# Performance work log

Measured on AMD Instinct MI355X. Metric: run time of the kernel, lower is better.

Reference implementation:

```python
import jax, jax.numpy as jnp
import numpy as np

B, T, D = 32, 2048, 80
K1 = K2 = 3
S1 = S2 = 2
CB_DIM, CB_SIZE = 512, 1024
MASK_P = 0.1
NOISE_STD = 0.1
INPUT_DIM = D * K1 * K2  # 720


def _win_idx(T_in, k, s):
    Tp = (T_in - k) // s + 1
    return jnp.arange(Tp)[:, None] * s + jnp.arange(k)[None, :]  # (Tp, k)


def _unfold(x, k, s):
    # matches torch x.unfold(1, k, s).view(B, Tp, -1): out[b, t, f*k + j] = x[b, t*s + j, f]
    idx = _win_idx(x.shape[1], k, s)
    w = x[:, idx, :]                 # (B, Tp, k, F)
    w = jnp.swapaxes(w, 2, 3)        # (B, Tp, F, k)
    return w.reshape(w.shape[0], w.shape[1], -1)


def setup_inputs() -> dict:
    key = jax.random.key(0)
    k1, k2, k3, k4, k5 = jax.random.split(key, 5)
    raw_feats = jax.random.normal(k1, (B, T, D), jnp.float32)
    auged_feats = jax.random.normal(k2, (B, T, D), jnp.float32)
    length = jax.random.randint(k3, (B,), T // 2, T + 1)
    xav = (2.0 / (INPUT_DIM + CB_DIM)) ** 0.5  # xavier_normal std
    projector = jax.random.normal(k4, (INPUT_DIM, CB_DIM), jnp.float32) * xav
    codebook = jax.random.normal(k5, (CB_SIZE, CB_DIM), jnp.float32)
    return {"raw_feats": raw_feats, "auged_feats": auged_feats, "length": length,
            "projector": projector, "codebook": codebook}


def reference(raw_feats, auged_feats, length, projector, codebook):
    T1 = (T - K1) // S1 + 1
    T2 = (T1 - K2) // S2 + 1
    idx1 = _win_idx(T, K1, S1)                         # (T1, K1)
    idx2 = _win_idx(T1, K2, S2)                        # (T2, K2)
    frame_windows = idx1[idx2].reshape(T2, K1 * K2)    # (T2, 9) original frame idx per subsampled step
    label_lengths = ((length - K1) // S1 + 1 - K2) // S2 + 1  # (B,)

    # --- label path: two torch-style unfolds -> project -> nearest codebook entry ---
    stacked = _unfold(_unfold(raw_feats, K1, S1), K2, S2)     # (B, T2, 720)
    targets = jnp.matmul(stacked, projector)                  # (B, T2, 512)
    # squared-euclidean expansion; same argmin as ||t - c||
    dist = (jnp.sum(targets * targets, axis=-1, keepdims=True)
            - 2.0 * jnp.einsum('btd,cd->btc', targets, codebook)
            + jnp.sum(codebook * codebook, axis=-1))          # (B, T2, 1024)
    labels = jnp.argmin(dist, axis=-1) + 1                    # labels start from 1; 0 = ignore idx
    valid = jnp.arange(T2)[None, :] < label_lengths[:, None]  # (B, T2)
    labels = jnp.where(valid, labels, 0)[None]                # (num_codebooks=1, B, T2)

    # --- static (span length 1) random masking on valid subsampled steps ---
    mkey = jax.random.key(42)
    km, kn = jax.random.split(mkey)
    masked = (jax.random.uniform(km, (B, T2)) < MASK_P) & valid
    masked_dim = masked.astype(jnp.float32)                   # (B, T2)
    # scatter masked subsampled steps back onto original frame indices (union of windows)
    hits = jnp.zeros((B, T), jnp.float32).at[:, frame_windows].add(masked_dim[:, :, None])
    frame_mask = hits > 0                                     # (B, T)
    noise = NOISE_STD * jax.random.normal(kn, (B, T, D), auged_feats.dtype)
    masked_feats = jnp.where(frame_mask[:, :, None], noise, auged_feats)
    return masked_feats, labels, masked_dim
```

## Files before the change

### kernel.cpp

```cpp
#include <hip/hip_runtime.h>
#include <cstdint>

#define B_    32
#define T_    2048
#define D_    80
#define T2_   511
#define NROW  16352
#define GK    720
#define CBD   512
#define CBS   1024
#define HMASK 8176
#define HN    2621440
#define NP    16384
#define KB    23
#define GLDS  (259*81*4)

using bfrag = __attribute__((ext_vector_type(8))) short;
using f32x4 = __attribute__((ext_vector_type(4))) float;
using s8    = __attribute__((ext_vector_type(8))) short;

__device__ inline ushort f2bf(float f){
  uint32_t u = __float_as_uint(f);
  uint32_t r = (u + 0x7FFFu + ((u >> 16) & 1u)) >> 16;
  return (ushort)r;
}
__device__ inline float bf2f(ushort h){ return __uint_as_float(((uint32_t)h) << 16); }

#define GLL16(gsrc, ldst) __builtin_amdgcn_global_load_lds( \
    (__attribute__((address_space(1))) void*)(gsrc), \
    (__attribute__((address_space(3))) void*)(ldst), 16, 0, 0)

__host__ __device__ inline uint32_t rotl_(uint32_t v, int d){ return (v<<d)|(v>>(32-d)); }

__host__ __device__ inline void tf2x32(uint32_t k0, uint32_t k1, uint32_t& x0, uint32_t& x1){
  uint32_t ks2 = k0 ^ k1 ^ 0x1BD11BDAu;
  x0 += k0; x1 += k1;
  const int r0[4] = {13,15,26,6}, r1[4] = {17,29,16,24};
#pragma unroll
  for (int i=0;i<4;i++){ x0 += x1; x1 = rotl_(x1, r0[i]); x1 ^= x0; }
  x0 += k1; x1 += ks2 + 1u;
#pragma unroll
  for (int i=0;i<4;i++){ x0 += x1; x1 = rotl_(x1, r1[i]); x1 ^= x0; }
  x0 += ks2; x1 += k0 + 2u;
#pragma unroll
  for (int i=0;i<4;i++){ x0 += x1; x1 = rotl_(x1, r0[i]); x1 ^= x0; }
  x0 += k0; x1 += k1 + 3u;
#pragma unroll
  for (int i=0;i<4;i++){ x0 += x1; x1 = rotl_(x1, r1[i]); x1 ^= x0; }
  x0 += k1; x1 += ks2 + 4u;
#pragma unroll
  for (int i=0;i<4;i++){ x0 += x1; x1 = rotl_(x1, r0[i]); x1 ^= x0; }
  x0 += ks2; x1 += k0 + 5u;
}

__device__ inline float erfinv_f(float x){
  float w = -log1pf(-x*x);
  float p;
  if (w < 5.0f){
    w -= 2.5f;
    p = 2.81022636e-08f;
    p = fmaf(p, w, 3.43273939e-07f);
    p = fmaf(p, w, -3.5233877e-06f);
    p = fmaf(p, w, -4.39150654e-06f);
    p = fmaf(p, w, 0.00021858087f);
    p = fmaf(p, w, -0.00125372503f);
    p = fmaf(p, w, -0.00417768164f);
    p = fmaf(p, w, 0.246640727f);
    p = fmaf(p, w, 1.50140941f);
  } else {
    w = sqrtf(w) - 3.0f;
    p = -0.000200214257f;
    p = fmaf(p, w, 0.000100950558f);
    p = fmaf(p, w, 0.00134934322f);
    p = fmaf(p, w, -0.00367342844f);
    p = fmaf(p, w, 0.00573950773f);
    p = fmaf(p, w, -0.0076224613f);
    p = fmaf(p, w, 0.00943887047f);
    p = fmaf(p, w, 1.00167406f);
    p = fmaf(p, w, 2.83297682f);
  }
  return p * x;
}

__device__ inline int label_len(int L){ return (((L - 3) / 2) - 2) / 2 + 1; }

__global__ void cbnorm_k(const float* __restrict__ cb, ushort* __restrict__ W0, ushort* __restrict__ W1){
  int c = blockIdx.x, lane = threadIdx.x;
  double s = 0.0;
  for (int k = lane; k < CBD; k += 64){ float v = cb[c*CBD + k]; s += (double)v * (double)v; }
#pragma unroll
  for (int off = 32; off; off >>= 1) s += __shfl_down(s, off);
  float nf = (float)s;
  nf = __shfl(nf, 0);
  size_t base = ((size_t)(KB-1)*CBS + c)*32;
  int sw = ((c >> 1) & 3) << 3;
  if (lane == 16){
    float h = -0.5f * nf;
    ushort h0 = f2bf(h); ushort h1 = f2bf(h - bf2f(h0));
    W0[base + (16 ^ sw)] = h0; W1[base + (16 ^ sw)] = h1;
  } else if (lane > 16 && lane < 32){
    W0[base + (lane ^ sw)] = 0; W1[base + (lane ^ sw)] = 0;
  }
}

__global__ __launch_bounds__(256) void gather_k(const float* __restrict__ raw,
                                                ushort* __restrict__ S0, ushort* __restrict__ S1){
  extern __shared__ float lraw[];
  int b = blockIdx.x >> 3, ch = blockIdx.x & 7;
  int t20 = ch * 64;
  int nt2 = (T2_ - t20 < 64) ? (T2_ - t20) : 64;
  int r0 = 4 * t20;
  int rows = (T_ - r0 < 259) ? (T_ - r0) : 259;
  int tid = threadIdx.x;
  const float4* gsrc = (const float4*)(raw + ((size_t)b*T_ + r0)*D_);
  int nf4 = rows * 20;
  for (int q = tid; q < nf4; q += 256){
    float4 v = gsrc[q];
    int row = q / 20, c4 = (q - row*20) * 4;
    float* dst = &lraw[row*81 + c4];
    dst[0]=v.x; dst[1]=v.y; dst[2]=v.z; dst[3]=v.w;
  }
  __syncthreads();
  int nl = tid >> 2, g = tid & 3;
  if (nl >= nt2) return;
  int n = b*T2_ + t20 + nl;
  int gs = g ^ ((n >> 1) & 3);
  for (int kb = 0; kb < KB; ++kb){
    s8 o0, o1;
#pragma unroll
    for (int j = 0; j < 8; ++j){
      int k = kb*32 + g*8 + j;
      float v = 0.f;
      if (k < GK){
        int d = k / 9, rem = k - 9*d;
        int k1 = rem / 3, k2 = rem - 3*k1;
        v = lraw[(4*nl + 2*k2 + k1)*81 + d];
      } else if (k == GK) v = 1.f;
      ushort h0 = f2bf(v); ushort h1 = f2bf(v - bf2f(h0));
      o0[j] = (short)h0; o1[j] = (short)h1;
    }
    size_t off = ((size_t)kb*NP + n)*32 + gs*8;
    *(s8*)&S0[off] = o0;
    *(s8*)&S1[off] = o1;
  }
}

__global__ __launch_bounds__(256) void wgemm_k(const float* __restrict__ P, const float* __restrict__ cb,
                                               float* __restrict__ Wp){
  __shared__ float sP[16][68];
  __shared__ float sC[16][68];
  int r0 = blockIdx.y * 64, c0 = blockIdx.x * 64;
  int kz = blockIdx.z;
  int tid = threadIdx.x, tx = tid & 15, ty = tid >> 4;
  float acc[4][4] = {};
  for (int k0 = kz * 128; k0 < kz * 128 + 128; k0 += 16){
    __syncthreads();
    {
      int r = tid >> 2, kq = tid & 3;
      int rr = r0 + r;
      float4 v = {0.f,0.f,0.f,0.f};
      if (rr < GK) v = *(const float4*)&P[rr * CBD + k0 + kq * 4];
      sP[kq*4+0][r] = v.x; sP[kq*4+1][r] = v.y; sP[kq*4+2][r] = v.z; sP[kq*4+3][r] = v.w;
      float4 w = *(const float4*)&cb[(c0 + r) * CBD + k0 + kq * 4];
      sC[kq*4+0][r] = w.x; sC[kq*4+1][r] = w.y; sC[kq*4+2][r] = w.z; sC[kq*4+3][r] = w.w;
    }
    __syncthreads();
#pragma unroll
    for (int kk = 0; kk < 16; ++kk){
      float4 a = *(const float4*)&sP[kk][ty * 4];
      float4 b = *(const float4*)&sC[kk][tx * 4];
      float av[4] = {a.x,a.y,a.z,a.w}, bv[4] = {b.x,b.y,b.z,b.w};
#pragma unroll
      for (int i = 0; i < 4; ++i)
#pragma unroll
        for (int j = 0; j < 4; ++j) acc[i][j] = fmaf(av[i], bv[j], acc[i][j]);
    }
  }
#pragma unroll
  for (int i = 0; i < 4; ++i){
    int r = r0 + ty * 4 + i;
    if (r < GK){
      float4 o; o.x = acc[i][0]; o.y = acc[i][1]; o.z = acc[i][2]; o.w = acc[i][3];
      *(float4*)&Wp[((size_t)kz * GK + r) * CBS + c0 + tx * 4] = o;
    }
  }
}

__global__ void wreduce_k(const float* __restrict__ Wp, ushort* __restrict__ W0, ushort* __restrict__ W1){
  int idx = blockIdx.x * 256 + threadIdx.x;
  int r = idx >> 10, c = idx & (CBS - 1);
  float v = Wp[(size_t)r * CBS + c]
          + Wp[((size_t)GK + r) * CBS + c]
          + Wp[((size_t)2*GK + r) * CBS + c]
          + Wp[((size_t)3*GK + r) * CBS + c];
  ushort h0 = f2bf(v); ushort h1 = f2bf(v - bf2f(h0));
  size_t o = ((size_t)(r >> 5) * CBS + c) * 32 + ((r & 31) ^ (((c >> 1) & 3) << 3));
  W0[o] = h0; W1[o] = h1;
}

__global__ __launch_bounds__(512, 2) void score_k(const ushort* __restrict__ S0, const ushort* __restrict__ S1,
                                                  const ushort* __restrict__ W0, const ushort* __restrict__ W1,
                                                  float* __restrict__ pval, int* __restrict__ pidx){
  extern __shared__ ushort lds[];
  int tid = threadIdx.x;
  int lane = tid & 63, wid = tid >> 6;
  int wm = wid >> 2, wn = wid & 3;
  int g = lane >> 4, lr = lane & 15;
  int gsw = g ^ ((lr >> 1) & 3);

  int id = blockIdx.x;
  int xcd = id & 7, slot = id >> 3;
  int cidx = slot & 3, ridx = (xcd << 3) | (slot >> 2);
  int n0 = ridx * 256, c0 = cidx * 256;

  int p = wid >> 1, h = wid & 1;
  const ushort* src0;
  size_t kstride;
  if      (p == 0){ src0 = S0 + (size_t)n0*32; kstride = (size_t)NP*32; }
  else if (p == 1){ src0 = S1 + (size_t)n0*32; kstride = (size_t)NP*32; }
  else if (p == 2){ src0 = W0 + (size_t)c0*32; kstride = (size_t)CBS*32; }
  else            { src0 = W1 + (size_t)c0*32; kstride = (size_t)CBS*32; }
  src0 += h * 4096;
  int doff = p * 8192 + h * 4096;

  f32x4 acc[8][4] = {};

#pragma unroll
  for (int q = 0; q < 8; ++q) GLL16(src0 + q*512 + lane*8, lds + doff + q*512);

  int abase = (wm*128 + lr)*32 + gsw*8;
  int bbase = (wn*64  + lr)*32 + gsw*8;

  for (int kb = 0; kb < KB; ++kb){
    const ushort* cur = lds + (kb & 1) * 32768;
    ushort*       nxt = lds + ((kb & 1) ^ 1) * 32768;
    asm volatile("s_waitcnt vmcnt(0)" ::: "memory");
    __builtin_amdgcn_s_barrier();

    const ushort* A0 = cur;
    const ushort* A1 = cur + 8192;
    const ushort* B0 = cur + 16384;
    const ushort* B1 = cur + 24576;

    bfrag a[4], b0f[4], b1f[4];
#pragma unroll
    for (int mt = 0; mt < 4; ++mt) a[mt] = *(const bfrag*)&A0[abase + mt*512];
#pragma unroll
    for (int nt = 0; nt < 4; ++nt) b0f[nt] = *(const bfrag*)&B0[bbase + nt*512];
    if (kb + 1 < KB){
      const ushort* s = src0 + (size_t)(kb+1)*kstride;
#pragma unroll
      for (int q = 0; q < 8; ++q) GLL16(s + q*512 + lane*8, nxt + doff + q*512);
    }
    asm volatile("s_waitcnt lgkmcnt(0)" ::: "memory");
    __builtin_amdgcn_sched_barrier(0);
    __builtin_amdgcn_s_setprio(1);
#pragma unroll
    for (int mt = 0; mt < 4; ++mt)
#pragma unroll
      for (int nt = 0; nt < 4; ++nt)
        acc[mt][nt] = __builtin_amdgcn_mfma_f32_16x16x32_bf16(a[mt], b0f[nt], acc[mt][nt], 0,0,0);
    __builtin_amdgcn_s_setprio(0);
    __builtin_amdgcn_sched_barrier(0);
    __builtin_amdgcn_s_barrier();
#pragma unroll
    for (int nt = 0; nt < 4; ++nt) b1f[nt] = *(const bfrag*)&B1[bbase + nt*512];
    asm volatile("s_waitcnt lgkmcnt(0)" ::: "memory");
    __builtin_amdgcn_sched_barrier(0);
    __builtin_amdgcn_s_setprio(1);
#pragma unroll
    for (int mt = 0; mt < 4; ++mt)
#pragma unroll
      for (int nt = 0; nt < 4; ++nt)
        acc[mt][nt] = __builtin_amdgcn_mfma_f32_16x16x32_bf16(a[mt], b1f[nt], acc[mt][nt], 0,0,0);
    __builtin_amdgcn_s_setprio(0);
    __builtin_amdgcn_sched_barrier(0);
    __builtin_amdgcn_s_barrier();
#pragma unroll
    for (int mt = 0; mt < 4; ++mt) a[mt] = *(const bfrag*)&A0[abase + (mt+4)*512];
    asm volatile("s_waitcnt lgkmcnt(0)" ::: "memory");
    __builtin_amdgcn_sched_barrier(0);
    __builtin_amdgcn_s_setprio(1);
#pragma unroll
    for (int mt = 0; mt < 4; ++mt)
#pragma unroll
      for (int nt = 0; nt < 4; ++nt)
        acc[4+mt][nt] = __builtin_amdgcn_mfma_f32_16x16x32_bf16(a[mt], b0f[nt], acc[4+mt][nt], 0,0,0);
#pragma unroll
    for (int mt = 0; mt < 4; ++mt)
#pragma unroll
      for (int nt = 0; nt < 4; ++nt)
        acc[4+mt][nt] = __builtin_amdgcn_mfma_f32_16x16x32_bf16(a[mt], b1f[nt], acc[4+mt][nt], 0,0,0);
    __builtin_amdgcn_s_setprio(0);
    __builtin_amdgcn_sched_barrier(0);
    __builtin_amdgcn_s_barrier();
    bfrag a1f[8];
#pragma unroll
    for (int mt = 0; mt < 8; ++mt) a1f[mt] = *(const bfrag*)&A1[abase + mt*512];
    asm volatile("s_waitcnt lgkmcnt(0)" ::: "memory");
    __builtin_amdgcn_sched_barrier(0);
    __builtin_amdgcn_s_setprio(1);
#pragma unroll
    for (int mt = 0; mt < 8; ++mt)
#pragma unroll
      for (int nt = 0; nt < 4; ++nt)
        acc[mt][nt] = __builtin_amdgcn_mfma_f32_16x16x32_bf16(a1f[mt], b0f[nt], acc[mt][nt], 0,0,0);
    __builtin_amdgcn_s_setprio(0);
    __builtin_amdgcn_sched_barrier(0);
  }

#pragma unroll
  for (int mt = 0; mt < 8; ++mt){
    float bv[4]; int bi[4];
#pragma unroll
    for (int r = 0; r < 4; ++r){
      float best = 3.4e38f; int besti = 0;
#pragma unroll
      for (int nt = 0; nt < 4; ++nt){
        float d = -2.f * acc[mt][nt][r];
        int c = c0 + wn*64 + nt*16 + lr;
        if (d < best){ best = d; besti = c; }
      }
      bv[r] = best; bi[r] = besti;
    }
#pragma unroll
    for (int off = 1; off < 16; off <<= 1){
#pragma unroll
      for (int r = 0; r < 4; ++r){
        float ov = __shfl_xor(bv[r], off);
        int   oi = __shfl_xor(bi[r], off);
        if (ov < bv[r] || (ov == bv[r] && oi < bi[r])){ bv[r] = ov; bi[r] = oi; }
      }
    }
    if (lr == 0){
      int pp = cidx*4 + wn;
#pragma unroll
      for (int r = 0; r < 4; ++r){
        int n = n0 + wm*128 + mt*16 + g*4 + r;
        pval[(size_t)pp*NP + n] = bv[r];
        pidx[(size_t)pp*NP + n] = bi[r];
      }
    }
  }
}

__device__ inline void emit_mask(const int* len, float* md, int i, uint32_t bits){
  float u = __uint_as_float((bits >> 9) | 0x3F800000u) - 1.0f;
  int b = i / T2_, t2 = i - b * T2_;
  bool m = (u < 0.1f) && (t2 < label_len(len[b]));
  md[i] = m ? 1.0f : 0.0f;
}

__device__ inline void comb_one(const float* __restrict__ pval, const int* __restrict__ pidx,
                                const int* __restrict__ len, float* __restrict__ lb, int n){
  float bv = pval[n]; int bi = pidx[n];
#pragma unroll
  for (int p = 1; p < 16; ++p){
    float v = pval[(size_t)p*NP + n]; int ii = pidx[(size_t)p*NP + n];
    if (v < bv || (v == bv && ii < bi)){ bv = v; bi = ii; }
  }
  int b = n / T2_, t2 = n - b * T2_;
  lb[n] = (t2 < label_len(len[b])) ? (float)(bi + 1) : 0.f;
}

__global__ void maskcomb_k(const float* __restrict__ pval, const int* __restrict__ pidx,
                           const int* __restrict__ len, float* __restrict__ lb,
                           float* __restrict__ md, uint32_t km0, uint32_t km1){
  int j = blockIdx.x * 256 + threadIdx.x;
  if (j >= HMASK) return;
  uint32_t x0 = (uint32_t)j, x1 = (uint32_t)(j + HMASK);
  tf2x32(km0, km1, x0, x1);
  emit_mask(len, md, j, x0);
  emit_mask(len, md, j + HMASK, x1);
  comb_one(pval, pidx, len, lb, j);
  comb_one(pval, pidx, len, lb, j + HMASK);
}

__device__ inline bool frame_masked(const float* md, int i){
  int tabs = i / D_;
  int t = tabs & (T_ - 1);
  int b = i / (D_ * T_);
  int lo = (t < 3) ? 0 : ((t - 3) >> 2);
  int hi = t >> 2; if (hi > T2_ - 1) hi = T2_ - 1;
  bool m = false;
  for (int t2 = lo; t2 <= hi; ++t2) m = m || (md[b * T2_ + t2] != 0.f);
  return m;
}

__device__ inline float noise_from_bits(uint32_t bits){
  float f = __uint_as_float((bits >> 9) | 0x3F800000u) - 1.0f;
  const float LOV = -0.99999994f;
  float u = fmaf(f, 2.0f, LOV);
  u = fmaxf(LOV, u);
  return 0.1f * (1.41421356f * erfinv_f(u));
}

__global__ void feats_k(const float* __restrict__ aug, const float* __restrict__ md,
                        float* __restrict__ mf, uint32_t kn0, uint32_t kn1){
  int j = blockIdx.x * 256 + threadIdx.x;
  bool m1 = frame_masked(md, j);
  bool m2 = frame_masked(md, j + HN);
  if (m1 || m2){
    uint32_t x0 = (uint32_t)j, x1 = (uint32_t)(j + HN);
    tf2x32(kn0, kn1, x0, x1);
    mf[j]      = m1 ? noise_from_bits(x0) : aug[j];
    mf[j + HN] = m2 ? noise_from_bits(x1) : aug[j + HN];
  } else {
    mf[j]      = aug[j];
    mf[j + HN] = aug[j + HN];
  }
}

extern "C" void kernel_launch(void* const* d_in, const int* in_sizes, int n_in,
                              void* d_out, int out_size, void* d_ws, size_t ws_size,
                              hipStream_t stream){
  const float* raw  = (const float*)d_in[0];
  const float* aug  = (const float*)d_in[1];
  const int*   len  = (const int*)  d_in[2];
  const float* proj = (const float*)d_in[3];
  const float* cb   = (const float*)d_in[4];

  float* out = (float*)d_out;
  float* mf  = out;
  float* lb  = out + 5242880;
  float* md  = out + 5259232;

  ushort* w  = (ushort*)d_ws;
  ushort* W0 = w;
  ushort* W1 = W0 + (size_t)KB*CBS*32;
  ushort* S0 = W1 + (size_t)KB*CBS*32;
  ushort* S1 = S0 + (size_t)KB*NP*32;
  float* pval = (float*)(S1 + (size_t)KB*NP*32);
  int*   pidx = (int*)(pval + (size_t)16*NP);
  float* Wp   = (float*)(pidx + (size_t)16*NP);

  hipFuncSetAttribute((const void*)score_k,  hipFuncAttributeMaxDynamicSharedMemorySize, 131072);
  hipFuncSetAttribute((const void*)gather_k, hipFuncAttributeMaxDynamicSharedMemorySize, GLDS);

  uint32_t a0 = 0u, a1 = 2u, b0 = 1u, b1 = 3u;
  tf2x32(0u, 42u, a0, a1);
  tf2x32(0u, 42u, b0, b1);
  uint32_t km0 = a0, km1 = b0, kn0 = a1, kn1 = b1;

  cbnorm_k<<<CBS, 64, 0, stream>>>(cb, W0, W1);
  wgemm_k<<<dim3(CBS / 64, 12, 4), 256, 0, stream>>>(proj, cb, Wp);
  wreduce_k<<<(GK * CBS) / 256, 256, 0, stream>>>(Wp, W0, W1);
  gather_k<<<256, 256, GLDS, stream>>>(raw, S0, S1);
  score_k<<<256, 512, 131072, stream>>>(S0, S1, W0, W1, pval, pidx);
  maskcomb_k<<<(HMASK + 255) / 256, 256, 0, stream>>>(pval, pidx, len, lb, md, km0, km1);
  feats_k<<<HN / 256, 256, 0, stream>>>(aug, md, mf, kn0, kn1);
}
```

Baseline: 147.8 us.

## Restructure score_k pipeline with early prefetch and fold cbnorm into wreduce

The codebook-norm kernel is merged into wreduce_k as extra blocks, removing one kernel launch. In score_k, the next k-block's global-to-LDS prefetch is now issued at the top of each iteration, followed by a partial vmcnt wait. The per-phase barriers and lgkmcnt waits between MFMA groups are dropped, so LDS fragment reads interleave with the MFMA groups. This aims to overlap memory loads with compute and cut synchronisation stalls. It risks relying on the compiler to insert correct LDS waits and on the partial vmcnt count staying correct.

```diff
diff --git a/kernel.cpp b/kernel.cpp
--- a/kernel.cpp
+++ b/kernel.cpp
@@ -84,25 +84,6 @@
 
 __device__ inline int label_len(int L){ return (((L - 3) / 2) - 2) / 2 + 1; }
 
-__global__ void cbnorm_k(const float* __restrict__ cb, ushort* __restrict__ W0, ushort* __restrict__ W1){
-  int c = blockIdx.x, lane = threadIdx.x;
-  double s = 0.0;
-  for (int k = lane; k < CBD; k += 64){ float v = cb[c*CBD + k]; s += (double)v * (double)v; }
-#pragma unroll
-  for (int off = 32; off; off >>= 1) s += __shfl_down(s, off);
-  float nf = (float)s;
-  nf = __shfl(nf, 0);
-  size_t base = ((size_t)(KB-1)*CBS + c)*32;
-  int sw = ((c >> 1) & 3) << 3;
-  if (lane == 16){
-    float h = -0.5f * nf;
-    ushort h0 = f2bf(h); ushort h1 = f2bf(h - bf2f(h0));
-    W0[base + (16 ^ sw)] = h0; W1[base + (16 ^ sw)] = h1;
-  } else if (lane > 16 && lane < 32){
-    W0[base + (lane ^ sw)] = 0; W1[base + (lane ^ sw)] = 0;
-  }
-}
-
 __global__ __launch_bounds__(256) void gather_k(const float* __restrict__ raw,
                                                 ushort* __restrict__ S0, ushort* __restrict__ S1){
   extern __shared__ float lraw[];
@@ -186,16 +167,38 @@
   }
 }
 
-__global__ void wreduce_k(const float* __restrict__ Wp, ushort* __restrict__ W0, ushort* __restrict__ W1){
-  int idx = blockIdx.x * 256 + threadIdx.x;
-  int r = idx >> 10, c = idx & (CBS - 1);
-  float v = Wp[(size_t)r * CBS + c]
-          + Wp[((size_t)GK + r) * CBS + c]
-          + Wp[((size_t)2*GK + r) * CBS + c]
-          + Wp[((size_t)3*GK + r) * CBS + c];
-  ushort h0 = f2bf(v); ushort h1 = f2bf(v - bf2f(h0));
-  size_t o = ((size_t)(r >> 5) * CBS + c) * 32 + ((r & 31) ^ (((c >> 1) & 3) << 3));
-  W0[o] = h0; W1[o] = h1;
+__global__ void wreduce_k(const float* __restrict__ Wp, const float* __restrict__ cb,
+                          ushort* __restrict__ W0, ushort* __restrict__ W1){
+  int bid = blockIdx.x;
+  if (bid < (GK * CBS) / 256){
+    int idx = bid * 256 + threadIdx.x;
+    int r = idx >> 10, c = idx & (CBS - 1);
+    float v = Wp[(size_t)r * CBS + c]
+            + Wp[((size_t)GK + r) * CBS + c]
+            + Wp[((size_t)2*GK + r) * CBS + c]
+            + Wp[((size_t)3*GK + r) * CBS + c];
+    ushort h0 = f2bf(v); ushort h1 = f2bf(v - bf2f(h0));
+    size_t o = ((size_t)(r >> 5) * CBS + c) * 32 + ((r & 31) ^ (((c >> 1) & 3) << 3));
+    W0[o] = h0; W1[o] = h1;
+  } else {
+    int c = (bid - (GK * CBS) / 256) * 4 + (threadIdx.x >> 6);
+    int lane = threadIdx.x & 63;
+    double s = 0.0;
+    for (int k = lane; k < CBD; k += 64){ float v = cb[c*CBD + k]; s += (double)v * (double)v; }
+#pragma unroll
+    for (int off = 32; off; off >>= 1) s += __shfl_down(s, off);
+    float nf = (float)s;
+    nf = __shfl(nf, 0);
+    size_t base = ((size_t)(KB-1)*CBS + c)*32;
+    int sw = ((c >> 1) & 3) << 3;
+    if (lane == 16){
+      float h = -0.5f * nf;
+      ushort h0 = f2bf(h); ushort h1 = f2bf(h - bf2f(h0));
+      W0[base + (16 ^ sw)] = h0; W1[base + (16 ^ sw)] = h1;
+    } else if (lane > 16 && lane < 32){
+      W0[base + (lane ^ sw)] = 0; W1[base + (lane ^ sw)] = 0;
+    }
+  }
 }
 
 __global__ __launch_bounds__(512, 2) void score_k(const ushort* __restrict__ S0, const ushort* __restrict__ S1,
@@ -234,7 +237,16 @@
   for (int kb = 0; kb < KB; ++kb){
     const ushort* cur = lds + (kb & 1) * 32768;
     ushort*       nxt = lds + ((kb & 1) ^ 1) * 32768;
-    asm volatile("s_waitcnt vmcnt(0)" ::: "memory");
+
+    __builtin_amdgcn_s_barrier();
+    if (kb + 1 < KB){
+      const ushort* s = src0 + (size_t)(kb+1)*kstride;
+#pragma unroll
+      for (int q = 0; q < 8; ++q) GLL16(s + q*512 + lane*8, nxt + doff + q*512);
+      asm volatile("s_waitcnt vmcnt(8)" ::: "memory");
+    } else {
+      asm volatile("s_waitcnt vmcnt(0)" ::: "memory");
+    }
     __builtin_amdgcn_s_barrier();
 
     const ushort* A0 = cur;
@@ -242,69 +254,69 @@
     const ushort* B0 = cur + 16384;
     const ushort* B1 = cur + 24576;
 
-    bfrag a[4], b0f[4], b1f[4];
-#pragma unroll
-    for (int mt = 0; mt < 4; ++mt) a[mt] = *(const bfrag*)&A0[abase + mt*512];
+    bfrag a0lo[4], a0hi[4], a1lo[4], a1hi[4], b0f[4], b1f[4];
 #pragma unroll
     for (int nt = 0; nt < 4; ++nt) b0f[nt] = *(const bfrag*)&B0[bbase + nt*512];
-    if (kb + 1 < KB){
-      const ushort* s = src0 + (size_t)(kb+1)*kstride;
-#pragma unroll
-      for (int q = 0; q < 8; ++q) GLL16(s + q*512 + lane*8, nxt + doff + q*512);
-    }
-    asm volatile("s_waitcnt lgkmcnt(0)" ::: "memory");
-    __builtin_amdgcn_sched_barrier(0);
-    __builtin_amdgcn_s_setprio(1);
-#pragma unroll
-    for (int mt = 0; mt < 4; ++mt)
-#pragma unroll
-      for (int nt = 0; nt < 4; ++nt)
-        acc[mt][nt] = __builtin_amdgcn_mfma_f32_16x16x32_bf16(a[mt], b0f[nt], acc[mt][nt], 0,0,0);
-    __builtin_amdgcn_s_setprio(0);
-    __builtin_amdgcn_sched_barrier(0);
-    __builtin_amdgcn_s_barrier();
+#pragma unroll
+    for (int mt = 0; mt < 4; ++mt) a0lo[mt] = *(const bfrag*)&A0[abase + mt*512];
 #pragma unroll
     for (int nt = 0; nt < 4; ++nt) b1f[nt] = *(const bfrag*)&B1[bbase + nt*512];
-    asm volatile("s_waitcnt lgkmcnt(0)" ::: "memory");
-    __builtin_amdgcn_sched_barrier(0);
-    __builtin_amdgcn_s_setprio(1);
-#pragma unroll
-    for (int mt = 0; mt < 4; ++mt)
-#pragma unroll
-      for (int nt = 0; nt < 4; ++nt)
-        acc[mt][nt] = __builtin_amdgcn_mfma_f32_16x16x32_bf16(a[mt], b1f[nt], acc[mt][nt], 0,0,0);
-    __builtin_amdgcn_s_setprio(0);
-    __builtin_amdgcn_sched_barrier(0);
-    __builtin_amdgcn_s_barrier();
-#pragma unroll
-    for (int mt = 0; mt < 4; ++mt) a[mt] = *(const bfrag*)&A0[abase + (mt+4)*512];
-    asm volatile("s_waitcnt lgkmcnt(0)" ::: "memory");
-    __builtin_amdgcn_sched_barrier(0);
-    __builtin_amdgcn_s_setprio(1);
-#pragma unroll
-    for (int mt = 0; mt < 4; ++mt)
-#pragma unroll
-      for (int nt = 0; nt < 4; ++nt)
-        acc[4+mt][nt] = __builtin_amdgcn_mfma_f32_16x16x32_bf16(a[mt], b0f[nt], acc[4+mt][nt], 0,0,0);
-#pragma unroll
-    for (int mt = 0; mt < 4; ++mt)
-#pragma unroll
-      for (int nt = 0; nt < 4; ++nt)
-        acc[4+mt][nt] = __builtin_amdgcn_mfma_f32_16x16x32_bf16(a[mt], b1f[nt], acc[4+mt][nt], 0,0,0);
-    __builtin_amdgcn_s_setprio(0);
-    __builtin_amdgcn_sched_barrier(0);
-    __builtin_amdgcn_s_barrier();
-    bfrag a1f[8];
-#pragma unroll
-    for (int mt = 0; mt < 8; ++mt) a1f[mt] = *(const bfrag*)&A1[abase + mt*512];
-    asm volatile("s_waitcnt lgkmcnt(0)" ::: "memory");
-    __builtin_amdgcn_sched_barrier(0);
-    __builtin_amdgcn_s_setprio(1);
-#pragma unroll
-    for (int mt = 0; mt < 8; ++mt)
-#pragma unroll
-      for (int nt = 0; nt < 4; ++nt)
-        acc[mt][nt] = __builtin_amdgcn_mfma_f32_16x16x32_bf16(a1f[mt], b0f[nt], acc[mt][nt], 0,0,0);
+    __builtin_amdgcn_sched_barrier(0);
+    __builtin_amdgcn_s_setprio(1);
+#pragma unroll
+    for (int mt = 0; mt < 4; ++mt)
+#pragma unroll
+      for (int nt = 0; nt < 4; ++nt)
+        acc[mt][nt] = __builtin_amdgcn_mfma_f32_16x16x32_bf16(a0lo[mt], b0f[nt], acc[mt][nt], 0,0,0);
+    __builtin_amdgcn_s_setprio(0);
+    __builtin_amdgcn_sched_barrier(0);
+#pragma unroll
+    for (int mt = 0; mt < 4; ++mt) a1lo[mt] = *(const bfrag*)&A1[abase + mt*512];
+    __builtin_amdgcn_sched_barrier(0);
+    __builtin_amdgcn_s_setprio(1);
+#pragma unroll
+    for (int mt = 0; mt < 4; ++mt)
+#pragma unroll
+      for (int nt = 0; nt < 4; ++nt)
+        acc[mt][nt] = __builtin_amdgcn_mfma_f32_16x16x32_bf16(a0lo[mt], b1f[nt], acc[mt][nt], 0,0,0);
+    __builtin_amdgcn_s_setprio(0);
+    __builtin_amdgcn_sched_barrier(0);
+#pragma unroll
+    for (int mt = 0; mt < 4; ++mt) a0hi[mt] = *(const bfrag*)&A0[abase + (mt+4)*512];
+    __builtin_amdgcn_sched_barrier(0);
+    __builtin_amdgcn_s_setprio(1);
+#pragma unroll
+    for (int mt = 0; mt < 4; ++mt)
+#pragma unroll
+      for (int nt = 0; nt < 4; ++nt)
+        acc[mt][nt] = __builtin_amdgcn_mfma_f32_16x16x32_bf16(a1lo[mt], b0f[nt], acc[mt][nt], 0,0,0);
+    __builtin_amdgcn_s_setprio(0);
+    __builtin_amdgcn_sched_barrier(0);
+#pragma unroll
+    for (int mt = 0; mt < 4; ++mt) a1hi[mt] = *(const bfrag*)&A1[abase + (mt+4)*512];
+    __builtin_amdgcn_sched_barrier(0);
+    __builtin_amdgcn_s_setprio(1);
+#pragma unroll
+    for (int mt = 0; mt < 4; ++mt)
+#pragma unroll
+      for (int nt = 0; nt < 4; ++nt)
+        acc[4+mt][nt] = __builtin_amdgcn_mfma_f32_16x16x32_bf16(a0hi[mt], b0f[nt], acc[4+mt][nt], 0,0,0);
+    __builtin_amdgcn_s_setprio(0);
+    __builtin_amdgcn_sched_barrier(0);
+    __builtin_amdgcn_s_setprio(1);
+#pragma unroll
+    for (int mt = 0; mt < 4; ++mt)
+#pragma unroll
+      for (int nt = 0; nt < 4; ++nt)
+        acc[4+mt][nt] = __builtin_amdgcn_mfma_f32_16x16x32_bf16(a0hi[mt], b1f[nt], acc[4+mt][nt], 0,0,0);
+    __builtin_amdgcn_s_setprio(0);
+    __builtin_amdgcn_sched_barrier(0);
+    __builtin_amdgcn_s_setprio(1);
+#pragma unroll
+    for (int mt = 0; mt < 4; ++mt)
+#pragma unroll
+      for (int nt = 0; nt < 4; ++nt)
+        acc[4+mt][nt] = __builtin_amdgcn_mfma_f32_16x16x32_bf16(a1hi[mt], b0f[nt], acc[4+mt][nt], 0,0,0);
     __builtin_amdgcn_s_setprio(0);
     __builtin_amdgcn_sched_barrier(0);
   }
@@ -442,9 +454,8 @@
   tf2x32(0u, 42u, b0, b1);
   uint32_t km0 = a0, km1 = b0, kn0 = a1, kn1 = b1;
 
-  cbnorm_k<<<CBS, 64, 0, stream>>>(cb, W0, W1);
   wgemm_k<<<dim3(CBS / 64, 12, 4), 256, 0, stream>>>(proj, cb, Wp);
-  wreduce_k<<<(GK * CBS) / 256, 256, 0, stream>>>(Wp, W0, W1);
+  wreduce_k<<<(GK * CBS) / 256 + CBS / 4, 256, 0, stream>>>(Wp, cb, W0, W1);
   gather_k<<<256, 256, GLDS, stream>>>(raw, S0, S1);
   score_k<<<256, 512, 131072, stream>>>(S0, S1, W0, W1, pval, pidx);
   maskcomb_k<<<(HMASK + 255) / 256, 256, 0, stream>>>(pval, pidx, len, lb, md, km0, km1);
```

Result: no change. 145.7 us (-1.4%).
